# Performance work log

Measured on AMD Instinct MI355X. Metric: run time of the kernel, lower is better.

The kernel has to match this reference:

```python
import jax, jax.numpy as jnp
import numpy as np
import math

H = 2048; NH = 16; HD = 128; E = 8; K = 2; F = 8192; CAP_F = 1.25
B = 2; S = 2048

def _layernorm(x, scale, bias, eps=1e-5):
    m = jnp.mean(x, axis=-1, keepdims=True)
    v = jnp.var(x, axis=-1, keepdims=True)
    return (x - m) * jax.lax.rsqrt(v + eps) * scale + bias

def _rope(x):
    # x: [B, S, NH, HD]; half-split RoPE, theta=10000
    hd = x.shape[-1]
    pos = jnp.arange(x.shape[1], dtype=jnp.float32)
    freqs = 1.0 / (10000.0 ** (jnp.arange(0, hd // 2, dtype=jnp.float32) / (hd // 2)))
    ang = pos[:, None] * freqs[None, :]              # [S, HD/2]
    cos = jnp.cos(ang)[None, :, None, :]
    sin = jnp.sin(ang)[None, :, None, :]
    x1, x2 = jnp.split(x, 2, axis=-1)
    return jnp.concatenate([x1 * cos - x2 * sin, x1 * sin + x2 * cos], axis=-1)

def setup_inputs() -> dict:
    key = jax.random.key(0)
    ks = jax.random.split(key, 16)
    std = 0.02
    inp = {
        'hidden_states': jax.random.normal(ks[0], (B, S, H), jnp.float32),
        'attention_mask': jnp.ones((B, S), jnp.int32),
        'ln1_scale': jnp.ones((H,), jnp.float32), 'ln1_bias': jnp.zeros((H,), jnp.float32),
        'ln2_scale': jnp.ones((H,), jnp.float32), 'ln2_bias': jnp.zeros((H,), jnp.float32),
        'Wq': jax.random.normal(ks[1], (H, NH * HD), jnp.float32) * std,
        'Wk': jax.random.normal(ks[2], (H, NH * HD), jnp.float32) * std,
        'Wv': jax.random.normal(ks[3], (H, NH * HD), jnp.float32) * std,
        'Wo': jax.random.normal(ks[4], (NH * HD, H), jnp.float32) * std,
        'Wg': jax.random.normal(ks[5], (H, H), jnp.float32) * std,
        'bg': jnp.zeros((H,), jnp.float32),
        'ls_attn': jnp.full((H,), 0.1, jnp.float32),
        'ls_moe': jnp.full((H,), 0.1, jnp.float32),
        'router_w': jax.random.normal(ks[6], (H, E), jnp.float32) * std,
        'W1': jax.random.normal(ks[7], (E, H, F), jnp.float32) * std,
        'b1': jnp.zeros((E, F), jnp.float32),
        'W2': jax.random.normal(ks[8], (E, F, H), jnp.float32) * std,
        'b2': jnp.zeros((E, H), jnp.float32),
    }
    return inp

def _forward(hidden_states, attention_mask, ln1_scale, ln1_bias, ln2_scale, ln2_bias,
             Wq, Wk, Wv, Wo, Wg, bg, ls_attn, ls_moe, router_w, W1, b1, W2, b2):
    b, s, h = hidden_states.shape
    # ---- pre-norm MLA attention + residual ----
    xn = _layernorm(hidden_states, ln1_scale, ln1_bias)
    q = (xn @ Wq).reshape(b, s, NH, HD)
    k = (xn @ Wk).reshape(b, s, NH, HD)
    v = (xn @ Wv).reshape(b, s, NH, HD)
    q = _rope(q); k = _rope(k)
    scores = jnp.einsum('bqhd,bkhd->bhqk', q, k) / math.sqrt(HD)
    causal = jnp.tril(jnp.ones((s, s), bool))
    mask = causal[None, None, :, :] & (attention_mask[:, None, None, :] > 0)
    scores = jnp.where(mask, scores, -1e9)
    attn = jax.nn.softmax(scores, axis=-1)
    ctx = jnp.einsum('bhqk,bkhd->bqhd', attn, v).reshape(b, s, NH * HD)
    attn_out = ctx @ Wo
    attn_out = attn_out * jax.nn.sigmoid(xn @ Wg + bg)   # output gating
    attn_out = attn_out * ls_attn                         # layer scale
    hidden_states = hidden_states + attn_out
    # ---- pre-norm MoE FFN + residual ----
    xn2 = _layernorm(hidden_states, ln2_scale, ln2_bias)
    T = b * s
    x = xn2.reshape(T, h)
    logits = (x @ router_w).astype(jnp.float32)           # [T, E]
    probs = jax.nn.softmax(logits, axis=-1)
    gates, idx = jax.lax.top_k(probs, K)                  # [T, K]
    gates = gates / jnp.sum(gates, axis=-1, keepdims=True)
    cap = int(math.ceil(T * K / E * CAP_F))               # expert capacity
    e_flat = idx.reshape(T * K)
    g_flat = gates.reshape(T * K)
    oh = jax.nn.one_hot(e_flat, E, dtype=jnp.int32)       # [TK, E]
    pos = jnp.sum(jnp.cumsum(oh, axis=0) * oh, axis=-1) - 1
    keep = (pos < cap).astype(x.dtype)
    pos_c = jnp.clip(pos, 0, cap - 1)
    x_rep = jnp.repeat(x, K, axis=0)                      # [TK, H]
    buf = jnp.zeros((E, cap, h), x.dtype).at[e_flat, pos_c].add(x_rep * keep[:, None])
    hmid = jax.nn.gelu(jnp.einsum('ech,ehf->ecf', buf, W1) + b1[:, None, :])
    obuf = jnp.einsum('ecf,efh->ech', hmid, W2) + b2[:, None, :]
    tok = obuf[e_flat, pos_c] * (keep * g_flat)[:, None]  # [TK, H]
    moe_out = tok.reshape(T, K, h).sum(axis=1).reshape(b, s, h)
    moe_out = moe_out * ls_moe
    return hidden_states + moe_out

def reference(hidden_states, attention_mask, ln1_scale, ln1_bias, ln2_scale, ln2_bias,
              Wq, Wk, Wv, Wo, Wg, bg, ls_attn, ls_moe, router_w, W1, b1, W2, b2):
    return _forward(hidden_states, attention_mask, ln1_scale, ln1_bias, ln2_scale, ln2_bias,
                    Wq, Wk, Wv, Wo, Wg, bg, ls_attn, ls_moe, router_w, W1, b1, W2, b2)
```

## Files before the change

kernel.cpp:

```cpp
#include <hip/hip_runtime.h>
#include <hip/hip_fp16.h>

typedef _Float16 f16;
typedef _Float16 half8 __attribute__((ext_vector_type(8)));
typedef float floatx4 __attribute__((ext_vector_type(4)));

constexpr int kH  = 2048;
constexpr int kS  = 2048;
constexpr int kB  = 2;
constexpr int kT  = kB * kS;
constexpr int kNH = 16;
constexpr int kHD = 128;
constexpr int kE  = 8;
constexpr int kF  = 8192;
constexpr int kCAP = 1280;
constexpr int kTK = kT * 2;

__device__ __forceinline__ void gload16(const void* g, void* lds_) {
  __builtin_amdgcn_global_load_lds((const __attribute__((address_space(1))) void*)g,
                                   (__attribute__((address_space(3))) void*)lds_,
                                   16, 0, 0);
}

__device__ __forceinline__ void xcd_remap(int& bx, int& by, int& bz) {
  const int gx = gridDim.x, gy = gridDim.y;
  const int nwg = gx * gy * gridDim.z;
  int L = (bz * gy + by) * gx + bx;
  L = (L & 7) * (nwg >> 3) + (L >> 3);
  bz = L / (gx * gy);
  const int r = L - bz * gx * gy;
  by = r / gx;  bx = r - by * gx;
}

__global__ __launch_bounds__(256) void transpose_cvt(
    const float* __restrict__ src, f16* __restrict__ dst,
    int ldS, int ldD, long sZ, long dZ)
{
  __shared__ float tile[64][65];
  src += (long)blockIdx.z * sZ;
  dst += (long)blockIdx.z * dZ;
  const int kb = blockIdx.y * 64, nb = blockIdx.x * 64;
  const int tx = threadIdx.x & 15, ty = threadIdx.x >> 4;
#pragma unroll
  for (int i = 0; i < 4; i++) {
    const int r = ty + i * 16;
    const float4 v = *(const float4*)&src[(long)(kb + r) * ldS + nb + tx * 4];
    tile[r][tx * 4 + 0] = v.x; tile[r][tx * 4 + 1] = v.y;
    tile[r][tx * 4 + 2] = v.z; tile[r][tx * 4 + 3] = v.w;
  }
  __syncthreads();
#pragma unroll
  for (int i = 0; i < 4; i++) {
    const int n = ty + i * 16;
    union { f16 h[4]; unsigned long long u; } pk;
#pragma unroll
    for (int j = 0; j < 4; j++) pk.h[j] = (f16)tile[tx * 4 + j][n];
    *(unsigned long long*)&dst[(long)(nb + n) * ldD + kb + tx * 4] = pk.u;
  }
}

__global__ __launch_bounds__(256) void ln_kernel(
    const float* __restrict__ x, const float* __restrict__ sc,
    const float* __restrict__ bi, f16* __restrict__ o16, float* __restrict__ o32)
{
  const long row = blockIdx.x;
  const float* xr = x + row * kH;
  const int t = threadIdx.x;
  const float4 u = ((const float4*)xr)[t * 2];
  const float4 v = ((const float4*)xr)[t * 2 + 1];
  float s = u.x + u.y + u.z + u.w + v.x + v.y + v.z + v.w;
  float q = u.x*u.x + u.y*u.y + u.z*u.z + u.w*u.w + v.x*v.x + v.y*v.y + v.z*v.z + v.w*v.w;
#pragma unroll
  for (int m = 1; m < 64; m <<= 1) { s += __shfl_xor(s, m); q += __shfl_xor(q, m); }
  __shared__ float red_s[4], red_q[4];
  const int w = t >> 6, l = t & 63;
  if (l == 0) { red_s[w] = s; red_q[w] = q; }
  __syncthreads();
  s = red_s[0] + red_s[1] + red_s[2] + red_s[3];
  q = red_q[0] + red_q[1] + red_q[2] + red_q[3];
  const float mean = s * (1.f / kH);
  const float var = q * (1.f / kH) - mean * mean;
  const float rstd = rsqrtf(var + 1e-5f);
  const int c = t * 8;
  const float vals[8] = {u.x, u.y, u.z, u.w, v.x, v.y, v.z, v.w};
#pragma unroll
  for (int j = 0; j < 8; j++) {
    const float y = (vals[j] - mean) * rstd * sc[c + j] + bi[c + j];
    o16[row * kH + c + j] = (f16)y;
    if (o32 != nullptr) o32[row * kH + c + j] = y;
  }
}

#define STG(SRC, TILE, KC, PAR, MAT) { \
  const f16* s_ = (SRC) + (long)(TILE) * 64 + (KC) * 32; \
  char* d_ = lds + ((PAR) * 65536 + (MAT) * 32768 + (KC) * 16384) + ldsW; \
  gload16(s_, d_); \
  gload16(s_ + 128 * ldGl, d_ + 8192); }

#define MROW(MH, MM, AF) \
  acc[(MH)*4+(MM)][0] = __builtin_amdgcn_mfma_f32_16x16x32_f16(AF, bf0, acc[(MH)*4+(MM)][0], 0, 0, 0); \
  acc[(MH)*4+(MM)][1] = __builtin_amdgcn_mfma_f32_16x16x32_f16(AF, bf1, acc[(MH)*4+(MM)][1], 0, 0, 0); \
  acc[(MH)*4+(MM)][2] = __builtin_amdgcn_mfma_f32_16x16x32_f16(AF, bf2, acc[(MH)*4+(MM)][2], 0, 0, 0); \
  acc[(MH)*4+(MM)][3] = __builtin_amdgcn_mfma_f32_16x16x32_f16(AF, bf3, acc[(MH)*4+(MM)][3], 0, 0, 0);

#define PH(PAR, KC, MH, RB, STAGE_STMT, VM_STMT) { \
  const char* au_ = lds + ((PAR) * 65536 + (KC) * 16384); \
  const char* bu_ = lds + ((PAR) * 65536 + 32768 + (KC) * 16384); \
  af0 = *(const half8*)(au_ + afoff + (MH) * 4096 +    0); \
  af1 = *(const half8*)(au_ + afoff + (MH) * 4096 + 1024); \
  af2 = *(const half8*)(au_ + afoff + (MH) * 4096 + 2048); \
  af3 = *(const half8*)(au_ + afoff + (MH) * 4096 + 3072); \
  if (RB) { \
    bf0 = *(const half8*)(bu_ + bfoff +    0); \
    bf1 = *(const half8*)(bu_ + bfoff + 1024); \
    bf2 = *(const half8*)(bu_ + bfoff + 2048); \
    bf3 = *(const half8*)(bu_ + bfoff + 3072); \
  } \
  STAGE_STMT; \
  VM_STMT; \
  __builtin_amdgcn_sched_barrier(0); \
  __builtin_amdgcn_s_barrier(); \
  asm volatile("s_waitcnt lgkmcnt(0)" ::: "memory"); \
  __builtin_amdgcn_sched_barrier(0); \
  __builtin_amdgcn_s_setprio(1); \
  MROW(MH, 0, af0) MROW(MH, 1, af1) MROW(MH, 2, af2) MROW(MH, 3, af3) \
  __builtin_amdgcn_s_setprio(0); }

#define VM10 asm volatile("s_waitcnt vmcnt(10)" ::: "memory")
#define VM8  asm volatile("s_waitcnt vmcnt(8)" ::: "memory")
#define VM4  asm volatile("s_waitcnt vmcnt(4)" ::: "memory")
#define VM0  asm volatile("s_waitcnt vmcnt(0)" ::: "memory")
#define NOP (void)0

template <int EPI, bool SPLITK, bool XCD>
__global__ __launch_bounds__(512, 2) void gemm8p_kernel(
    const f16* __restrict__ A, const f16* __restrict__ B, void* __restrict__ Cv,
    const float* __restrict__ bias, const int* __restrict__ rowCount,
    int M, int N, int K, long ldA, long ldB, long aZ, long bZ, long cZ,
    long cZ2, long biasZ)
{
  int bx = blockIdx.x, by = blockIdx.y, bz = blockIdx.z;
  if (XCD) xcd_remap(bx, by, bz);
  const int z = bz;
  const int ze = SPLITK ? (z >> 1) : z;
  if (rowCount != nullptr && (int)(by * 256) >= rowCount[ze]) return;
  __shared__ __align__(16) char lds[131072];
  const long khoff = SPLITK ? (long)(z & 1) * K : 0;
  A += (long)ze * aZ + khoff;  B += (long)ze * bZ + khoff;
  const int tid = threadIdx.x, w = tid >> 6, l = tid & 63;
  const int g = l >> 4, lr = l & 15;
  const long m0 = (long)by * 256, n0 = (long)bx * 256;
  const int wm = (w >> 2) * 128, wn = (w & 3) * 64;

  floatx4 acc[8][4];
#pragma unroll
  for (int i = 0; i < 8; i++)
#pragma unroll
    for (int j = 0; j < 4; j++) acc[i][j] = floatx4{0.f, 0.f, 0.f, 0.f};

  const int swzS = ((l & 3) * 8) ^ (((l >> 3) & 3) << 3);
  const f16* aSrc;
  const f16* bSrc;
  long ldGl;
  {
    const int srow = w * 16 + (l >> 2);
    aSrc = A + (m0 + srow) * ldA + swzS;
    bSrc = B + (n0 + srow) * ldB + swzS;
  }
  ldGl = ldA;
  const int ldsW = w * 1024;
  const int rsw = (g * 16) ^ (((lr >> 1) & 3) << 4);
  const int afoff = wm * 64 + lr * 64 + rsw;
  const int bfoff = wn * 64 + lr * 64 + rsw;
  half8 af0, af1, af2, af3;
  half8 bf0 = half8{0}, bf1 = half8{0}, bf2 = half8{0}, bf3 = half8{0};

  STG(aSrc, 0, 0, 0, 0);
  STG(bSrc, 0, 0, 0, 1);
  STG(aSrc, 0, 1, 0, 0);
  STG(bSrc, 0, 1, 0, 1);
  STG(bSrc, 1, 0, 1, 1);
  STG(aSrc, 1, 0, 1, 0);
  STG(bSrc, 1, 1, 1, 1);
  VM10;
  __builtin_amdgcn_sched_barrier(0);
  __builtin_amdgcn_s_barrier();

  const int NI = K >> 7;
  for (int i = 0; i < NI - 1; i++) {
    const int t0 = 2 * i, t1 = 2 * i + 1;
    PH(0, 0, 0, 1, STG(aSrc, (t1),     1, 1, 0), VM10)
    PH(0, 0, 1, 0, STG(bSrc, (t0 + 2), 0, 0, 1), VM10)
    PH(0, 1, 0, 1, STG(aSrc, (t0 + 2), 0, 0, 0), VM10)
    PH(0, 1, 1, 0, STG(bSrc, (t0 + 2), 1, 0, 1), VM10)
    PH(1, 0, 0, 1, STG(aSrc, (t0 + 2), 1, 0, 0), VM10)
    PH(1, 0, 1, 0, STG(bSrc, (t1 + 2), 0, 1, 1), VM10)
    PH(1, 1, 0, 1, STG(aSrc, (t1 + 2), 0, 1, 0), VM10)
    PH(1, 1, 1, 0, STG(bSrc, (t1 + 2), 1, 1, 1), VM10)
  }
  {
    const int t1 = 2 * (NI - 1) + 1;
    PH(0, 0, 0, 1, STG(aSrc, (t1), 1, 1, 0), VM8)
    PH(0, 0, 1, 0, NOP, NOP)
    PH(0, 1, 0, 1, NOP, VM4)
    PH(0, 1, 1, 0, NOP, NOP)
    PH(1, 0, 0, 1, NOP, VM0)
    PH(1, 0, 1, 0, NOP, NOP)
    PH(1, 1, 0, 1, NOP, NOP)
    PH(1, 1, 1, 0, NOP, NOP)
  }

  const long crow = m0 + wm + g * 4;
  const long ccol = n0 + wn + lr;
  float* c32 = (float*)Cv + (long)ze * cZ + (SPLITK ? (long)(z & 1) * cZ2 : 0);
#pragma unroll
  for (int mi = 0; mi < 8; mi++)
#pragma unroll
    for (int ni = 0; ni < 4; ni++)
#pragma unroll
      for (int j = 0; j < 4; j++) {
        const long r = crow + mi * 16 + j;
        const long c = ccol + ni * 16;
        float v = acc[mi][ni][j];
        if (EPI == 0) {
          c32[r * N + c] = v;
        } else if (EPI == 2) {
          v += bias[(long)ze * biasZ + c];
          const float u2 = 1.5957691216057308f * (v + 0.044715f * v * v * v);
          const float sg = 1.f / (1.f + __expf(-u2));
          ((f16*)Cv)[(long)ze * cZ + r * N + c] = (f16)(v * sg);
        } else {
          v += bias[(long)ze * biasZ + c];
          ((f16*)Cv)[(long)ze * cZ + r * N + c] = (f16)v;
        }
      }
}
#undef STG
#undef MROW
#undef PH
#undef VM10
#undef VM8
#undef VM4
#undef VM0
#undef NOP

__global__ void rope_table_kernel(float* __restrict__ ct, float* __restrict__ st) {
  const int i = blockIdx.x * 256 + threadIdx.x;
  if (i >= kS * 64) return;
  const int s = i >> 6, f = i & 63;
  const double freq = exp(-0.14391156831212787 * (double)f);
  const double ang = (double)s * freq;
  ct[i] = (float)cos(ang);
  st[i] = (float)sin(ang);
}

__global__ __launch_bounds__(256) void rope_kernel(
    const float* __restrict__ q, const float* __restrict__ k,
    const float* __restrict__ ct, const float* __restrict__ st,
    f16* __restrict__ qr, f16* __restrict__ kr)
{
  const long t = blockIdx.x;
  const int s = (int)(t & (kS - 1)), b = (int)(t >> 11);
  for (int u = threadIdx.x; u < kNH * 64; u += 256) {
    const int h = u >> 6, i = u & 63;
    const float c = ct[s * 64 + i], sn = st[s * 64 + i];
    const long src = t * kH + h * kHD + i;
    const long dst = (((long)(b * kNH + h)) * kS + s) * kHD + i;
    float x1 = q[src], x2 = q[src + 64];
    qr[dst]      = (f16)((x1 * c - x2 * sn) * 0.08838834764831845f);
    qr[dst + 64] = (f16)((x1 * sn + x2 * c) * 0.08838834764831845f);
    x1 = k[src]; x2 = k[src + 64];
    kr[dst]      = (f16)(x1 * c - x2 * sn);
    kr[dst + 64] = (f16)(x1 * sn + x2 * c);
  }
}

__global__ __launch_bounds__(256) void attn_kernel(
    const f16* __restrict__ q_r, const f16* __restrict__ k_r,
    const f16* __restrict__ v_t, f16* __restrict__ ctx)
{
  __shared__ f16 Ks[64 * 128];
  __shared__ f16 Vs[128 * 64];
  __shared__ f16 Ps[4][1024];
  int qt = blockIdx.x, h = blockIdx.y, b = blockIdx.z;
  xcd_remap(qt, h, b);
  const int bh = b * kNH + h;
  const int tid = threadIdx.x, w = tid >> 6, l = tid & 63;
  const int g = l >> 4, lr = l & 15;
  const long q0 = (long)qt * 64;
  const f16* qbase = q_r + ((long)bh * kS + q0 + w * 16 + lr) * kHD;
  half8 qf[4];
#pragma unroll
  for (int kc = 0; kc < 4; kc++) qf[kc] = *(const half8*)(qbase + kc * 32 + g * 8);
  floatx4 acc[8];
#pragma unroll
  for (int i = 0; i < 8; i++) acc[i] = floatx4{0.f, 0.f, 0.f, 0.f};
  float mrun[4], lrun[4];
#pragma unroll
  for (int j = 0; j < 4; j++) { mrun[j] = -1e30f; lrun[j] = 0.f; }
  f16* pw = Ps[w];

  for (int kt = 0; kt <= qt; kt++) {
    const long k0 = (long)kt * 64;
#pragma unroll
    for (int c = 0; c < 4; c++) {
      const int cc = w * 4 + c;
      const int row = cc * 4 + (l >> 4);
      const int wb = (l & 15) * 16;
      const int src = (wb ^ ((row & 7) << 4)) >> 1;
      gload16(k_r + ((long)bh * kS + k0 + row) * kHD + src, Ks + cc * 512);
    }
#pragma unroll
    for (int c = 0; c < 4; c++) {
      const int cc = w * 4 + c;
      const int row = cc * 8 + (l >> 3);
      const int wb = (l & 7) * 16;
      const int src = (wb ^ ((row & 7) << 4)) >> 1;
      gload16(v_t + ((long)bh * kHD + row) * kS + k0 + src, Vs + cc * 512);
    }
    asm volatile("s_waitcnt vmcnt(0)" ::: "memory");
    __syncthreads();

    floatx4 sfr[4];
#pragma unroll
    for (int f = 0; f < 4; f++) {
      floatx4 s4 = floatx4{0.f, 0.f, 0.f, 0.f};
      const int row = f * 16 + lr;
#pragma unroll
      for (int kc = 0; kc < 4; kc++) {
        const half8 kfq = *(const half8*)((const char*)Ks + row * 256 +
                            ((kc * 64 + g * 16) ^ ((row & 7) << 4)));
        s4 = __builtin_amdgcn_mfma_f32_16x16x32_f16(qf[kc], kfq, s4, 0, 0, 0);
      }
      sfr[f] = s4;
    }
    if (kt == qt) {
#pragma unroll
      for (int f = 0; f < 4; f++) {
        const int key = kt * 64 + f * 16 + lr;
#pragma unroll
        for (int j = 0; j < 4; j++) {
          const int qrow = qt * 64 + w * 16 + g * 4 + j;
          if (key > qrow) sfr[f][j] = -1e30f;
        }
      }
    }
    float al[4];
#pragma unroll
    for (int j = 0; j < 4; j++) {
      float pm = fmaxf(fmaxf(sfr[0][j], sfr[1][j]), fmaxf(sfr[2][j], sfr[3][j]));
      pm = fmaxf(pm, __shfl_xor(pm, 1)); pm = fmaxf(pm, __shfl_xor(pm, 2));
      pm = fmaxf(pm, __shfl_xor(pm, 4)); pm = fmaxf(pm, __shfl_xor(pm, 8));
      const float mn = fmaxf(mrun[j], pm);
      al[j] = __expf(mrun[j] - mn);
      mrun[j] = mn;
      float rs = 0.f;
#pragma unroll
      for (int f = 0; f < 4; f++) {
        const float p = __expf(sfr[f][j] - mn);
        sfr[f][j] = p; rs += p;
      }
      rs += __shfl_xor(rs, 1); rs += __shfl_xor(rs, 2);
      rs += __shfl_xor(rs, 4); rs += __shfl_xor(rs, 8);
      lrun[j] = lrun[j] * al[j] + rs;
    }
#pragma unroll
    for (int nf = 0; nf < 8; nf++)
#pragma unroll
      for (int j = 0; j < 4; j++) acc[nf][j] *= al[j];
#pragma unroll
    for (int f = 0; f < 4; f++)
#pragma unroll
      for (int j = 0; j < 4; j++) {
        const int row = g * 4 + j;
        const int byteoff = (row * 128 + (f * 16 + lr) * 2) ^ ((row & 7) << 4);
        *(f16*)((char*)pw + byteoff) = (f16)sfr[f][j];
      }
#pragma unroll
    for (int kc = 0; kc < 2; kc++) {
      const half8 pf = *(const half8*)((const char*)pw + lr * 128 +
                         ((kc * 64 + g * 16) ^ ((lr & 7) << 4)));
#pragma unroll
      for (int nf = 0; nf < 8; nf++) {
        const int vrow = nf * 16 + lr;
        const half8 vfr = *(const half8*)((const char*)Vs + vrow * 128 +
                            ((kc * 64 + g * 16) ^ ((vrow & 7) << 4)));
        acc[nf] = __builtin_amdgcn_mfma_f32_16x16x32_f16(pf, vfr, acc[nf], 0, 0, 0);
      }
    }
    __syncthreads();
  }
  const long orow = (long)b * kS + q0 + w * 16;
#pragma unroll
  for (int j = 0; j < 4; j++) {
    const float inv = 1.0f / lrun[j];
    const int r = g * 4 + j;
#pragma unroll
    for (int nf = 0; nf < 8; nf++)
      ctx[(orow + r) * kH + h * kHD + nf * 16 + lr] = (f16)(acc[nf][j] * inv);
  }
}

__global__ __launch_bounds__(256) void combine1_kernel(
    const float* __restrict__ hid, const float* __restrict__ a0,
    const float* __restrict__ a1, const float* __restrict__ glin,
    const float* __restrict__ bg, const float* __restrict__ ls,
    float* __restrict__ out)
{
  const long i = (long)blockIdx.x * 256 + threadIdx.x;
  const float4 hv = ((const float4*)hid)[i];
  const float4 av = ((const float4*)a0)[i];
  const float4 aw = ((const float4*)a1)[i];
  const float4 gv = ((const float4*)glin)[i];
  const int c = (int)(i & 511);
  const float4 lv = ((const float4*)ls)[c];
  const float4 bv = ((const float4*)bg)[c];
  float4 o;
  o.x = hv.x + lv.x * (av.x + aw.x) / (1.f + __expf(-(gv.x + bv.x)));
  o.y = hv.y + lv.y * (av.y + aw.y) / (1.f + __expf(-(gv.y + bv.y)));
  o.z = hv.z + lv.z * (av.z + aw.z) / (1.f + __expf(-(gv.z + bv.z)));
  o.w = hv.w + lv.w * (av.w + aw.w) / (1.f + __expf(-(gv.w + bv.w)));
  ((float4*)out)[i] = o;
}

__global__ __launch_bounds__(256) void router_kernel(
    const float* __restrict__ x, const float* __restrict__ rw,
    int* __restrict__ eidx, float* __restrict__ gates)
{
  const int t = blockIdx.x * 4 + (threadIdx.x >> 6);
  const int l = threadIdx.x & 63;
  const float* xr = x + (long)t * kH;
  float a[8] = {0.f, 0.f, 0.f, 0.f, 0.f, 0.f, 0.f, 0.f};
  for (int it = 0; it < kH / 64; it++) {
    const float xv = xr[it * 64 + l];
    const float* r = rw + (long)(it * 64 + l) * kE;
#pragma unroll
    for (int e = 0; e < 8; e++) a[e] += xv * r[e];
  }
#pragma unroll
  for (int e = 0; e < 8; e++)
#pragma unroll
    for (int m = 1; m < 64; m <<= 1) a[e] += __shfl_xor(a[e], m);
  if (l == 0) {
    float mx = a[0];
#pragma unroll
    for (int e = 1; e < 8; e++) mx = fmaxf(mx, a[e]);
    float p[8];
#pragma unroll
    for (int e = 0; e < 8; e++) p[e] = __expf(a[e] - mx);
    int i1 = 0; float v1 = p[0];
#pragma unroll
    for (int e = 1; e < 8; e++) if (p[e] > v1) { v1 = p[e]; i1 = e; }
    int i2 = -1; float v2 = -1.f;
#pragma unroll
    for (int e = 0; e < 8; e++) if (e != i1 && p[e] > v2) { v2 = p[e]; i2 = e; }
    const float inv = 1.f / (v1 + v2);
    eidx[t * 2] = i1; eidx[t * 2 + 1] = i2;
    gates[t * 2] = v1 * inv; gates[t * 2 + 1] = v2 * inv;
  }
}

__global__ void scan_kernel(const int* __restrict__ eidx, int* __restrict__ slot,
                            int* __restrict__ counts)
{
  const int l = threadIdx.x;
  int base[8] = {0, 0, 0, 0, 0, 0, 0, 0};
  const unsigned long long lt = (1ull << l) - 1ull;
  for (int it = 0; it < kTK / 64; it++) {
    const int i = it * 64 + l;
    const int e = eidx[i];
    int mypos = 0;
#pragma unroll
    for (int ex = 0; ex < 8; ex++) {
      const unsigned long long mk = __ballot(e == ex);
      if (e == ex) mypos = base[ex] + __popcll(mk & lt);
      base[ex] += __popcll(mk);
    }
    slot[i] = (mypos < kCAP) ? e * kCAP + mypos : -1;
  }
  if (l == 0) {
#pragma unroll
    for (int ex = 0; ex < 8; ex++) counts[ex] = min(base[ex], kCAP);
  }
}

__global__ __launch_bounds__(256) void scatter_kernel(
    const f16* __restrict__ xh, const int* __restrict__ slot, f16* __restrict__ buf)
{
  const int i = blockIdx.x;
  const int s = slot[i];
  if (s < 0) return;
  const long t = i >> 1;
  ((half8*)(buf + (long)s * kH))[threadIdx.x] =
      ((const half8*)(xh + t * kH))[threadIdx.x];
}

__global__ __launch_bounds__(256) void combine2_kernel(
    const float* __restrict__ hid2, const float* __restrict__ P0,
    const float* __restrict__ P1, const int* __restrict__ slot,
    const float* __restrict__ gates, const float* __restrict__ b2,
    const float* __restrict__ ls, float* __restrict__ out)
{
  const int t = blockIdx.x;
  const int c = threadIdx.x * 8;
  float m[8] = {0.f, 0.f, 0.f, 0.f, 0.f, 0.f, 0.f, 0.f};
#pragma unroll
  for (int ks = 0; ks < 2; ks++) {
    const int s = slot[t * 2 + ks];
    if (s < 0) continue;
    const float gte = gates[t * 2 + ks];
    const int e = s / kCAP;
    const long ro = (long)s * kH + c;
    const float4 p0a = *(const float4*)&P0[ro];
    const float4 p0b = *(const float4*)&P0[ro + 4];
    const float4 p1a = *(const float4*)&P1[ro];
    const float4 p1b = *(const float4*)&P1[ro + 4];
    const float4 ba = *(const float4*)&b2[e * kH + c];
    const float4 bb = *(const float4*)&b2[e * kH + c + 4];
    m[0] += gte * (p0a.x + p1a.x + ba.x);
    m[1] += gte * (p0a.y + p1a.y + ba.y);
    m[2] += gte * (p0a.z + p1a.z + ba.z);
    m[3] += gte * (p0a.w + p1a.w + ba.w);
    m[4] += gte * (p0b.x + p1b.x + bb.x);
    m[5] += gte * (p0b.y + p1b.y + bb.y);
    m[6] += gte * (p0b.z + p1b.z + bb.z);
    m[7] += gte * (p0b.w + p1b.w + bb.w);
  }
  const float* hp = hid2 + (long)t * kH + c;
  float* op = out + (long)t * kH + c;
#pragma unroll
  for (int j = 0; j < 8; j++) op[j] = hp[j] + ls[c + j] * m[j];
}

extern "C" void kernel_launch(void* const* d_in, const int* in_sizes, int n_in,
                              void* d_out, int out_size, void* d_ws, size_t ws_size,
                              hipStream_t stream)
{
  (void)in_sizes; (void)n_in;
  const float* hidden   = (const float*)d_in[0];
  const float* ln1s     = (const float*)d_in[2];
  const float* ln1b     = (const float*)d_in[3];
  const float* ln2s     = (const float*)d_in[4];
  const float* ln2b     = (const float*)d_in[5];
  const float* Wq       = (const float*)d_in[6];
  const float* Wk       = (const float*)d_in[7];
  const float* Wv       = (const float*)d_in[8];
  const float* Wo       = (const float*)d_in[9];
  const float* Wg       = (const float*)d_in[10];
  const float* bg       = (const float*)d_in[11];
  const float* ls_attn  = (const float*)d_in[12];
  const float* ls_moe   = (const float*)d_in[13];
  const float* router_w = (const float*)d_in[14];
  const float* W1       = (const float*)d_in[15];
  const float* b1       = (const float*)d_in[16];
  const float* W2       = (const float*)d_in[17];
  const float* b2       = (const float*)d_in[18];

  char* ws = (char*)d_ws;
  size_t off = 0;
  auto take = [&](size_t b) { size_t r = off; off += (b + 255) & ~(size_t)255; return r; };
  const size_t o_wT   = take(5ULL * kH * kH * 2);
  const size_t o_w1t  = take((size_t)kE * kF * kH * 2);
  const size_t o_w2t  = take((size_t)kE * kH * kF * 2);
  const size_t o_xn   = take((size_t)kT * kH * 2);
  const size_t o_qkvg = take(4ULL * kT * kH * 4);
  const size_t o_tab  = take(2ULL * kS * 64 * 4);
  const size_t o_qr   = take(3ULL * kT * kH * 2);
  const size_t o_ctx  = take((size_t)kT * kH * 2);
  const size_t o_h2   = take((size_t)kT * kH * 4);
  const size_t o_sm   = take(1 << 20);
  const size_t o_hmid = take((size_t)kE * kCAP * kF * 2);
  if (off > ws_size) { hipMemsetAsync(d_out, 0xFF, (size_t)out_size * 4, stream); return; }

  f16* wT    = (f16*)(ws + o_wT);
  f16* w1t   = (f16*)(ws + o_w1t);
  f16* w2t   = (f16*)(ws + o_w2t);
  f16* xn    = (f16*)(ws + o_xn);
  float* qf  = (float*)(ws + o_qkvg);
  float* kfp = qf + (size_t)kT * kH;
  float* vfp = kfp + (size_t)kT * kH;
  float* gfp = vfp + (size_t)kT * kH;
  float* tabc = (float*)(ws + o_tab);
  float* tabs = tabc + (size_t)kS * 64;
  f16* qr  = (f16*)(ws + o_qr);
  f16* kr  = qr + (size_t)kT * kH;
  f16* vt  = kr + (size_t)kT * kH;
  f16* ctx = (f16*)(ws + o_ctx);
  float* h2 = (float*)(ws + o_h2);
  int* eidx    = (int*)(ws + o_sm);
  float* gates = (float*)(ws + o_sm + 65536);
  int* slot    = (int*)(ws + o_sm + 131072);
  int* counts  = (int*)(ws + o_sm + 196608);
  f16* hmid = (f16*)(ws + o_hmid);
  float* x2f = vfp;
  f16* x2h  = (f16*)(ws + o_qkvg + 1ULL * kT * kH * 4 + (size_t)kT * kH * 2);
  f16* buf  = qr;
  float* woP0 = qf;
  float* woP1 = kfp;
  float* P0 = (float*)(ws + o_qkvg);
  float* P1 = (float*)(ws + o_w1t);
  const long pStride = (long)(P1 - P0);

  const long HH = (long)kH * kH;

  transpose_cvt<<<dim3(32, 32, 1), 256, 0, stream>>>(Wq, wT + 0 * HH, kH, kH, 0, 0);
  transpose_cvt<<<dim3(32, 32, 1), 256, 0, stream>>>(Wk, wT + 1 * HH, kH, kH, 0, 0);
  transpose_cvt<<<dim3(32, 32, 1), 256, 0, stream>>>(Wv, wT + 2 * HH, kH, kH, 0, 0);
  transpose_cvt<<<dim3(32, 32, 1), 256, 0, stream>>>(Wg, wT + 3 * HH, kH, kH, 0, 0);
  transpose_cvt<<<dim3(32, 32, 1), 256, 0, stream>>>(Wo, wT + 4 * HH, kH, kH, 0, 0);
  transpose_cvt<<<dim3(kF / 64, kH / 64, kE), 256, 0, stream>>>(
      W1, w1t, kF, kH, (long)kH * kF, (long)kF * kH);
  transpose_cvt<<<dim3(kH / 64, kF / 64, kE), 256, 0, stream>>>(
      W2, w2t, kH, kF, (long)kF * kH, (long)kH * kF);
  ln_kernel<<<kT, 256, 0, stream>>>(hidden, ln1s, ln1b, xn, nullptr);
  gemm8p_kernel<0, false, true><<<dim3(kH / 256, kT / 256, 4), 512, 0, stream>>>(
      xn, wT, qf, nullptr, nullptr, kT, kH, kH, kH, kH,
      0L, HH, (long)kT * kH, 0L, 0L);
  rope_table_kernel<<<(kS * 64 + 255) / 256, 256, 0, stream>>>(tabc, tabs);
  rope_kernel<<<kT, 256, 0, stream>>>(qf, kfp, tabc, tabs, qr, kr);
  for (int b = 0; b < kB; b++)
    transpose_cvt<<<dim3(kHD / 64, kS / 64, kNH), 256, 0, stream>>>(
        vfp + (size_t)b * kS * kH, vt + (size_t)b * kNH * kHD * kS,
        kH, kS, 128L, (long)kHD * kS);
  attn_kernel<<<dim3(kS / 64, kNH, kB), 256, 0, stream>>>(qr, kr, vt, ctx);
  gemm8p_kernel<0, true, true><<<dim3(kH / 256, kT / 256, 2), 512, 0, stream>>>(
      ctx, wT + 4 * HH, woP0, nullptr, nullptr, kT, kH, 1024, kH, kH,
      0L, 0L, 0L, (long)kT * kH, 0L);
  combine1_kernel<<<(kT * kH / 4) / 256, 256, 0, stream>>>(
      hidden, woP0, woP1, gfp, bg, ls_attn, h2);
  ln_kernel<<<kT, 256, 0, stream>>>(h2, ln2s, ln2b, x2h, x2f);
  router_kernel<<<kT / 4, 256, 0, stream>>>(x2f, router_w, eidx, gates);
  scan_kernel<<<1, 64, 0, stream>>>(eidx, slot, counts);
  scatter_kernel<<<kTK, 256, 0, stream>>>(x2h, slot, buf);
  gemm8p_kernel<2, false, false><<<dim3(kF / 256, kCAP / 256, kE), 512, 0, stream>>>(
      buf, w1t, hmid, b1, counts, kCAP, kF, kH, kH, kH,
      (long)kCAP * kH, (long)kF * kH, (long)kCAP * kF, 0L, (long)kF);
  gemm8p_kernel<0, true, false><<<dim3(kH / 256, kCAP / 256, 2 * kE), 512, 0, stream>>>(
      hmid, w2t, P0, nullptr, counts, kCAP, kH, 4096, kF, kF,
      (long)kCAP * kF, (long)kH * kF, (long)kCAP * kH, pStride, 0L);
  combine2_kernel<<<kT, 256, 0, stream>>>(
      h2, P0, P1, slot, gates, b2, ls_moe, (float*)d_out);
}
```

Measured before the change: 1.566 ms.

## Widen attention tile to 128 queries and store split-K partials as fp16

Attention blocks now handle 128 query rows each, two 16-row fragments per wave, so every K/V tile loaded into shared memory feeds twice as many MFMAs. MFMA sections are wrapped with s_setprio. The split-K partial outputs of the Wo and W2 GEMMs are written as fp16 through a new epilogue, and the combine kernels read them as fp16, halving that write and read traffic. This costs precision in the partial sums and doubles register and LDS use per block in attention, which may reduce occupancy.

Result: slower. 1.601 ms (+2.2%).

```diff
diff --git a/kernel.cpp b/kernel.cpp
--- a/kernel.cpp
+++ b/kernel.cpp
@@ -2,6 +2,7 @@
 #include <hip/hip_fp16.h>
 
 typedef _Float16 f16;
+typedef _Float16 half4 __attribute__((ext_vector_type(4)));
 typedef _Float16 half8 __attribute__((ext_vector_type(8)));
 typedef float floatx4 __attribute__((ext_vector_type(4)));
 
@@ -213,6 +214,7 @@
   const long crow = m0 + wm + g * 4;
   const long ccol = n0 + wn + lr;
   float* c32 = (float*)Cv + (long)ze * cZ + (SPLITK ? (long)(z & 1) * cZ2 : 0);
+  f16* ch = (f16*)Cv + (long)ze * cZ + (SPLITK ? (long)(z & 1) * cZ2 : 0);
 #pragma unroll
   for (int mi = 0; mi < 8; mi++)
 #pragma unroll
@@ -229,9 +231,11 @@
           const float u2 = 1.5957691216057308f * (v + 0.044715f * v * v * v);
           const float sg = 1.f / (1.f + __expf(-u2));
           ((f16*)Cv)[(long)ze * cZ + r * N + c] = (f16)(v * sg);
-        } else {
+        } else if (EPI == 3) {
           v += bias[(long)ze * biasZ + c];
           ((f16*)Cv)[(long)ze * cZ + r * N + c] = (f16)v;
+        } else {
+          ch[r * N + c] = (f16)v;
         }
       }
 }
@@ -281,26 +285,34 @@
 {
   __shared__ f16 Ks[64 * 128];
   __shared__ f16 Vs[128 * 64];
-  __shared__ f16 Ps[4][1024];
+  __shared__ f16 Ps[4][2048];
   int qt = blockIdx.x, h = blockIdx.y, b = blockIdx.z;
   xcd_remap(qt, h, b);
   const int bh = b * kNH + h;
   const int tid = threadIdx.x, w = tid >> 6, l = tid & 63;
   const int g = l >> 4, lr = l & 15;
-  const long q0 = (long)qt * 64;
-  const f16* qbase = q_r + ((long)bh * kS + q0 + w * 16 + lr) * kHD;
-  half8 qf[4];
-#pragma unroll
-  for (int kc = 0; kc < 4; kc++) qf[kc] = *(const half8*)(qbase + kc * 32 + g * 8);
-  floatx4 acc[8];
-#pragma unroll
-  for (int i = 0; i < 8; i++) acc[i] = floatx4{0.f, 0.f, 0.f, 0.f};
-  float mrun[4], lrun[4];
-#pragma unroll
-  for (int j = 0; j < 4; j++) { mrun[j] = -1e30f; lrun[j] = 0.f; }
+  const long q0 = (long)qt * 128;
+  half8 qf[2][4];
+#pragma unroll
+  for (int f2 = 0; f2 < 2; f2++) {
+    const f16* qb = q_r + ((long)bh * kS + q0 + w * 32 + f2 * 16 + lr) * kHD;
+#pragma unroll
+    for (int kc = 0; kc < 4; kc++) qf[f2][kc] = *(const half8*)(qb + kc * 32 + g * 8);
+  }
+  floatx4 acc[2][8];
+#pragma unroll
+  for (int f2 = 0; f2 < 2; f2++)
+#pragma unroll
+    for (int i = 0; i < 8; i++) acc[f2][i] = floatx4{0.f, 0.f, 0.f, 0.f};
+  float mrun[2][4], lrun[2][4];
+#pragma unroll
+  for (int f2 = 0; f2 < 2; f2++)
+#pragma unroll
+    for (int j = 0; j < 4; j++) { mrun[f2][j] = -1e30f; lrun[f2][j] = 0.f; }
   f16* pw = Ps[w];
 
-  for (int kt = 0; kt <= qt; kt++) {
+  const int ktEnd = 2 * qt + 1;
+  for (int kt = 0; kt <= ktEnd; kt++) {
     const long k0 = (long)kt * 64;
 #pragma unroll
     for (int c = 0; c < 4; c++) {
@@ -321,105 +333,118 @@
     asm volatile("s_waitcnt vmcnt(0)" ::: "memory");
     __syncthreads();
 
-    floatx4 sfr[4];
-#pragma unroll
-    for (int f = 0; f < 4; f++) {
-      floatx4 s4 = floatx4{0.f, 0.f, 0.f, 0.f};
-      const int row = f * 16 + lr;
-#pragma unroll
-      for (int kc = 0; kc < 4; kc++) {
-        const half8 kfq = *(const half8*)((const char*)Ks + row * 256 +
-                            ((kc * 64 + g * 16) ^ ((row & 7) << 4)));
-        s4 = __builtin_amdgcn_mfma_f32_16x16x32_f16(qf[kc], kfq, s4, 0, 0, 0);
+#pragma unroll
+    for (int f2 = 0; f2 < 2; f2++) {
+      floatx4 sfr[4];
+      __builtin_amdgcn_s_setprio(1);
+#pragma unroll
+      for (int f = 0; f < 4; f++) {
+        floatx4 s4 = floatx4{0.f, 0.f, 0.f, 0.f};
+        const int row = f * 16 + lr;
+#pragma unroll
+        for (int kc = 0; kc < 4; kc++) {
+          const half8 kfq = *(const half8*)((const char*)Ks + row * 256 +
+                              ((kc * 64 + g * 16) ^ ((row & 7) << 4)));
+          s4 = __builtin_amdgcn_mfma_f32_16x16x32_f16(qf[f2][kc], kfq, s4, 0, 0, 0);
+        }
+        sfr[f] = s4;
       }
-      sfr[f] = s4;
-    }
-    if (kt == qt) {
-#pragma unroll
-      for (int f = 0; f < 4; f++) {
-        const int key = kt * 64 + f * 16 + lr;
-#pragma unroll
-        for (int j = 0; j < 4; j++) {
-          const int qrow = qt * 64 + w * 16 + g * 4 + j;
-          if (key > qrow) sfr[f][j] = -1e30f;
+      __builtin_amdgcn_s_setprio(0);
+      if (kt >= 2 * qt) {
+#pragma unroll
+        for (int f = 0; f < 4; f++) {
+          const int key = kt * 64 + f * 16 + lr;
+#pragma unroll
+          for (int j = 0; j < 4; j++) {
+            const int qrow = qt * 128 + w * 32 + f2 * 16 + g * 4 + j;
+            if (key > qrow) sfr[f][j] = -1e30f;
+          }
         }
       }
+#pragma unroll
+      for (int j = 0; j < 4; j++) {
+        float pm = fmaxf(fmaxf(sfr[0][j], sfr[1][j]), fmaxf(sfr[2][j], sfr[3][j]));
+        pm = fmaxf(pm, __shfl_xor(pm, 1)); pm = fmaxf(pm, __shfl_xor(pm, 2));
+        pm = fmaxf(pm, __shfl_xor(pm, 4)); pm = fmaxf(pm, __shfl_xor(pm, 8));
+        const float mn = fmaxf(mrun[f2][j], pm);
+        const float al = __expf(mrun[f2][j] - mn);
+        mrun[f2][j] = mn;
+        float rs = 0.f;
+#pragma unroll
+        for (int f = 0; f < 4; f++) {
+          const float p = __expf(sfr[f][j] - mn);
+          sfr[f][j] = p; rs += p;
+        }
+        rs += __shfl_xor(rs, 1); rs += __shfl_xor(rs, 2);
+        rs += __shfl_xor(rs, 4); rs += __shfl_xor(rs, 8);
+        lrun[f2][j] = lrun[f2][j] * al + rs;
+#pragma unroll
+        for (int nf = 0; nf < 8; nf++) acc[f2][nf][j] *= al;
+      }
+#pragma unroll
+      for (int f = 0; f < 4; f++)
+#pragma unroll
+        for (int j = 0; j < 4; j++) {
+          const int row = f2 * 16 + g * 4 + j;
+          const int byteoff = (row * 128 + (f * 16 + lr) * 2) ^ ((row & 7) << 4);
+          *(f16*)((char*)pw + byteoff) = (f16)sfr[f][j];
+        }
     }
-    float al[4];
-#pragma unroll
-    for (int j = 0; j < 4; j++) {
-      float pm = fmaxf(fmaxf(sfr[0][j], sfr[1][j]), fmaxf(sfr[2][j], sfr[3][j]));
-      pm = fmaxf(pm, __shfl_xor(pm, 1)); pm = fmaxf(pm, __shfl_xor(pm, 2));
-      pm = fmaxf(pm, __shfl_xor(pm, 4)); pm = fmaxf(pm, __shfl_xor(pm, 8));
-      const float mn = fmaxf(mrun[j], pm);
-      al[j] = __expf(mrun[j] - mn);
-      mrun[j] = mn;
-      float rs = 0.f;
-#pragma unroll
-      for (int f = 0; f < 4; f++) {
-        const float p = __expf(sfr[f][j] - mn);
-        sfr[f][j] = p; rs += p;
+    __builtin_amdgcn_s_setprio(1);
+#pragma unroll
+    for (int kc = 0; kc < 2; kc++) {
+      half8 pf0, pf1;
+      {
+        const int p0r = lr, p1r = 16 + lr;
+        pf0 = *(const half8*)((const char*)pw + p0r * 128 +
+                ((kc * 64 + g * 16) ^ ((p0r & 7) << 4)));
+        pf1 = *(const half8*)((const char*)pw + p1r * 128 +
+                ((kc * 64 + g * 16) ^ ((p1r & 7) << 4)));
       }
-      rs += __shfl_xor(rs, 1); rs += __shfl_xor(rs, 2);
-      rs += __shfl_xor(rs, 4); rs += __shfl_xor(rs, 8);
-      lrun[j] = lrun[j] * al[j] + rs;
-    }
-#pragma unroll
-    for (int nf = 0; nf < 8; nf++)
-#pragma unroll
-      for (int j = 0; j < 4; j++) acc[nf][j] *= al[j];
-#pragma unroll
-    for (int f = 0; f < 4; f++)
-#pragma unroll
-      for (int j = 0; j < 4; j++) {
-        const int row = g * 4 + j;
-        const int byteoff = (row * 128 + (f * 16 + lr) * 2) ^ ((row & 7) << 4);
-        *(f16*)((char*)pw + byteoff) = (f16)sfr[f][j];
-      }
-#pragma unroll
-    for (int kc = 0; kc < 2; kc++) {
-      const half8 pf = *(const half8*)((const char*)pw + lr * 128 +
-                         ((kc * 64 + g * 16) ^ ((lr & 7) << 4)));
 #pragma unroll
       for (int nf = 0; nf < 8; nf++) {
         const int vrow = nf * 16 + lr;
         const half8 vfr = *(const half8*)((const char*)Vs + vrow * 128 +
                             ((kc * 64 + g * 16) ^ ((vrow & 7) << 4)));
-        acc[nf] = __builtin_amdgcn_mfma_f32_16x16x32_f16(pf, vfr, acc[nf], 0, 0, 0);
+        acc[0][nf] = __builtin_amdgcn_mfma_f32_16x16x32_f16(pf0, vfr, acc[0][nf], 0, 0, 0);
+        acc[1][nf] = __builtin_amdgcn_mfma_f32_16x16x32_f16(pf1, vfr, acc[1][nf], 0, 0, 0);
       }
     }
+    __builtin_amdgcn_s_setprio(0);
     __syncthreads();
   }
-  const long orow = (long)b * kS + q0 + w * 16;
-#pragma unroll
-  for (int j = 0; j < 4; j++) {
-    const float inv = 1.0f / lrun[j];
-    const int r = g * 4 + j;
-#pragma unroll
-    for (int nf = 0; nf < 8; nf++)
-      ctx[(orow + r) * kH + h * kHD + nf * 16 + lr] = (f16)(acc[nf][j] * inv);
-  }
+  const long orow = (long)b * kS + q0 + w * 32;
+#pragma unroll
+  for (int f2 = 0; f2 < 2; f2++)
+#pragma unroll
+    for (int j = 0; j < 4; j++) {
+      const float inv = 1.0f / lrun[f2][j];
+      const int r = f2 * 16 + g * 4 + j;
+#pragma unroll
+      for (int nf = 0; nf < 8; nf++)
+        ctx[(orow + r) * kH + h * kHD + nf * 16 + lr] = (f16)(acc[f2][nf][j] * inv);
+    }
 }
 
 __global__ __launch_bounds__(256) void combine1_kernel(
-    const float* __restrict__ hid, const float* __restrict__ a0,
-    const float* __restrict__ a1, const float* __restrict__ glin,
+    const float* __restrict__ hid, const f16* __restrict__ a0,
+    const f16* __restrict__ a1, const float* __restrict__ glin,
     const float* __restrict__ bg, const float* __restrict__ ls,
     float* __restrict__ out)
 {
   const long i = (long)blockIdx.x * 256 + threadIdx.x;
   const float4 hv = ((const float4*)hid)[i];
-  const float4 av = ((const float4*)a0)[i];
-  const float4 aw = ((const float4*)a1)[i];
+  const half4 av = ((const half4*)a0)[i];
+  const half4 aw = ((const half4*)a1)[i];
   const float4 gv = ((const float4*)glin)[i];
   const int c = (int)(i & 511);
   const float4 lv = ((const float4*)ls)[c];
   const float4 bv = ((const float4*)bg)[c];
   float4 o;
-  o.x = hv.x + lv.x * (av.x + aw.x) / (1.f + __expf(-(gv.x + bv.x)));
-  o.y = hv.y + lv.y * (av.y + aw.y) / (1.f + __expf(-(gv.y + bv.y)));
-  o.z = hv.z + lv.z * (av.z + aw.z) / (1.f + __expf(-(gv.z + bv.z)));
-  o.w = hv.w + lv.w * (av.w + aw.w) / (1.f + __expf(-(gv.w + bv.w)));
+  o.x = hv.x + lv.x * ((float)av[0] + (float)aw[0]) / (1.f + __expf(-(gv.x + bv.x)));
+  o.y = hv.y + lv.y * ((float)av[1] + (float)aw[1]) / (1.f + __expf(-(gv.y + bv.y)));
+  o.z = hv.z + lv.z * ((float)av[2] + (float)aw[2]) / (1.f + __expf(-(gv.z + bv.z)));
+  o.w = hv.w + lv.w * ((float)av[3] + (float)aw[3]) / (1.f + __expf(-(gv.w + bv.w)));
   ((float4*)out)[i] = o;
 }
 
@@ -496,8 +521,8 @@
 }
 
 __global__ __launch_bounds__(256) void combine2_kernel(
-    const float* __restrict__ hid2, const float* __restrict__ P0,
-    const float* __restrict__ P1, const int* __restrict__ slot,
+    const float* __restrict__ hid2, const f16* __restrict__ P0,
+    const f16* __restrict__ P1, const int* __restrict__ slot,
     const float* __restrict__ gates, const float* __restrict__ b2,
     const float* __restrict__ ls, float* __restrict__ out)
 {
@@ -511,20 +536,18 @@
     const float gte = gates[t * 2 + ks];
     const int e = s / kCAP;
     const long ro = (long)s * kH + c;
-    const float4 p0a = *(const float4*)&P0[ro];
-    const float4 p0b = *(const float4*)&P0[ro + 4];
-    const float4 p1a = *(const float4*)&P1[ro];
-    const float4 p1b = *(const float4*)&P1[ro + 4];
+    const half8 p0 = *(const half8*)&P0[ro];
+    const half8 p1 = *(const half8*)&P1[ro];
     const float4 ba = *(const float4*)&b2[e * kH + c];
     const float4 bb = *(const float4*)&b2[e * kH + c + 4];
-    m[0] += gte * (p0a.x + p1a.x + ba.x);
-    m[1] += gte * (p0a.y + p1a.y + ba.y);
-    m[2] += gte * (p0a.z + p1a.z + ba.z);
-    m[3] += gte * (p0a.w + p1a.w + ba.w);
-    m[4] += gte * (p0b.x + p1b.x + bb.x);
-    m[5] += gte * (p0b.y + p1b.y + bb.y);
-    m[6] += gte * (p0b.z + p1b.z + bb.z);
-    m[7] += gte * (p0b.w + p1b.w + bb.w);
+    m[0] += gte * ((float)p0[0] + (float)p1[0] + ba.x);
+    m[1] += gte * ((float)p0[1] + (float)p1[1] + ba.y);
+    m[2] += gte * ((float)p0[2] + (float)p1[2] + ba.z);
+    m[3] += gte * ((float)p0[3] + (float)p1[3] + ba.w);
+    m[4] += gte * ((float)p0[4] + (float)p1[4] + bb.x);
+    m[5] += gte * ((float)p0[5] + (float)p1[5] + bb.y);
+    m[6] += gte * ((float)p0[6] + (float)p1[6] + bb.z);
+    m[7] += gte * ((float)p0[7] + (float)p1[7] + bb.w);
   }
   const float* hp = hid2 + (long)t * kH + c;
   float* op = out + (long)t * kH + c;
@@ -595,11 +618,9 @@
   float* x2f = vfp;
   f16* x2h  = (f16*)(ws + o_qkvg + 1ULL * kT * kH * 4 + (size_t)kT * kH * 2);
   f16* buf  = qr;
-  float* woP0 = qf;
-  float* woP1 = kfp;
-  float* P0 = (float*)(ws + o_qkvg);
-  float* P1 = (float*)(ws + o_w1t);
-  const long pStride = (long)(P1 - P0);
+  f16* woPh = (f16*)qf;
+  f16* P0h = (f16*)(ws + o_w1t);
+  f16* P1h = P0h + (size_t)kE * kCAP * kH;
 
   const long HH = (long)kH * kH;
 
@@ -622,12 +643,12 @@
     transpose_cvt<<<dim3(kHD / 64, kS / 64, kNH), 256, 0, stream>>>(
         vfp + (size_t)b * kS * kH, vt + (size_t)b * kNH * kHD * kS,
         kH, kS, 128L, (long)kHD * kS);
-  attn_kernel<<<dim3(kS / 64, kNH, kB), 256, 0, stream>>>(qr, kr, vt, ctx);
-  gemm8p_kernel<0, true, true><<<dim3(kH / 256, kT / 256, 2), 512, 0, stream>>>(
-      ctx, wT + 4 * HH, woP0, nullptr, nullptr, kT, kH, 1024, kH, kH,
+  attn_kernel<<<dim3(kS / 128, kNH, kB), 256, 0, stream>>>(qr, kr, vt, ctx);
+  gemm8p_kernel<4, true, true><<<dim3(kH / 256, kT / 256, 2), 512, 0, stream>>>(
+      ctx, wT + 4 * HH, woPh, nullptr, nullptr, kT, kH, 1024, kH, kH,
       0L, 0L, 0L, (long)kT * kH, 0L);
   combine1_kernel<<<(kT * kH / 4) / 256, 256, 0, stream>>>(
-      hidden, woP0, woP1, gfp, bg, ls_attn, h2);
+      hidden, woPh, woPh + (size_t)kT * kH, gfp, bg, ls_attn, h2);
   ln_kernel<<<kT, 256, 0, stream>>>(h2, ln2s, ln2b, x2h, x2f);
   router_kernel<<<kT / 4, 256, 0, stream>>>(x2f, router_w, eidx, gates);
   scan_kernel<<<1, 64, 0, stream>>>(eidx, slot, counts);
@@ -635,9 +656,9 @@
   gemm8p_kernel<2, false, false><<<dim3(kF / 256, kCAP / 256, kE), 512, 0, stream>>>(
       buf, w1t, hmid, b1, counts, kCAP, kF, kH, kH, kH,
       (long)kCAP * kH, (long)kF * kH, (long)kCAP * kF, 0L, (long)kF);
-  gemm8p_kernel<0, true, false><<<dim3(kH / 256, kCAP / 256, 2 * kE), 512, 0, stream>>>(
-      hmid, w2t, P0, nullptr, counts, kCAP, kH, 4096, kF, kF,
-      (long)kCAP * kF, (long)kH * kF, (long)kCAP * kH, pStride, 0L);
+  gemm8p_kernel<4, true, false><<<dim3(kH / 256, kCAP / 256, 2 * kE), 512, 0, stream>>>(
+      hmid, w2t, P0h, nullptr, counts, kCAP, kH, 4096, kF, kF,
+      (long)kCAP * kF, (long)kH * kF, (long)kCAP * kH, (long)kE * kCAP * kH, 0L);
   combine2_kernel<<<kT, 256, 0, stream>>>(
-      h2, P0, P1, slot, gates, b2, ls_moe, (float*)d_out);
-}
+      h2, P0h, P1h, slot, gates, b2, ls_moe, (float*)d_out);
+}
```
